# Kernel optimization log

Hardware: AMD Instinct MI355X
Metric: run time of the kernel (lower is better)

Reference implementation:

```python
import jax, jax.numpy as jnp
import numpy as np
import math

B, N, C_IN, C_OUT, K, RATIO = 16, 4096, 256, 512, 16, 0.25
N_OUT = math.ceil(N * RATIO)  # 1024
BN_EPS = 1e-5


def fps_indices(p, n):
    """Farthest point sampling. p: [B,N,3] -> local indices [B,n] (deterministic start at 0, eval mode)."""
    def fps_one(pts):  # [N,3]
        d0 = jnp.sum((pts - pts[0]) ** 2, axis=-1)          # [N]
        idxs0 = jnp.zeros((n,), jnp.int32)                  # idx[0] = 0
        def body(i, st):
            d, idxs = st
            nxt = jnp.argmax(d).astype(jnp.int32)
            idxs = idxs.at[i].set(nxt)
            d = jnp.minimum(d, jnp.sum((pts - pts[nxt]) ** 2, axis=-1))
            return (d, idxs)
        _, idxs = jax.lax.fori_loop(1, n, body, (d0, idxs0))
        return idxs
    return jax.vmap(fps_one)(p)


def setup_inputs() -> dict:
    key = jax.random.key(0)
    ks = jax.random.split(key, 6)
    x = jax.random.normal(ks[0], (B, N, C_IN), jnp.float32)
    p = jax.random.normal(ks[1], (B, N, 3), jnp.float32)
    sid_euc = jax.random.randint(ks[2], (B * N, K), 0, B * N).astype(jnp.int64)
    tid_euc = jax.random.randint(ks[3], (B * N, K), 0, B * N).astype(jnp.int64)
    W = jax.random.normal(ks[4], (C_OUT, C_IN), jnp.float32) * (1.0 / np.sqrt(C_IN))
    b = jax.random.normal(ks[5], (C_OUT,), jnp.float32) * 0.02
    gamma = jnp.ones((C_OUT,), jnp.float32)
    beta = jnp.zeros((C_OUT,), jnp.float32)
    run_mean = jnp.zeros((C_OUT,), jnp.float32)
    run_var = jnp.ones((C_OUT,), jnp.float32)
    return {"x": x, "p": p, "sid_euc": sid_euc, "tid_euc": tid_euc,
            "W": W, "b": b, "gamma": gamma, "beta": beta,
            "run_mean": run_mean, "run_var": run_var}


def reference(x, p, sid_euc, tid_euc, W, b, gamma, beta, run_mean, run_var):
    Bsz, Npts, _ = x.shape
    n = N_OUT
    Kn = sid_euc.shape[1]
    # MLP: pointwise Linear + BatchNorm (eval) + ReLU
    h = jnp.einsum('bnc,oc->bno', x, W) + b                       # [B,N,C_OUT]
    h = (h - run_mean) * (gamma / jnp.sqrt(run_var + BN_EPS)) + beta
    h = jax.nn.relu(h)
    # FPS -> global flat indices into B*N
    fid_local = fps_indices(p, n)                                  # [B,n]
    fid = (fid_local + jnp.arange(Bsz, dtype=jnp.int32)[:, None] * Npts).reshape(-1)
    # sample coords
    p_flat = p.reshape(Bsz * Npts, -1)
    p_out = p_flat[fid].reshape(Bsz, n, -1)                        # [B,n,3]
    # gather K neighbors of each sampled point, max-pool over K
    sid = sid_euc[fid].reshape(-1)                                 # [B*n*K]
    h_flat = h.reshape(Bsz * Npts, -1)
    x_out = h_flat[sid].reshape(Bsz, n, Kn, -1).max(axis=-2)       # [B,n,C_OUT]
    return (x_out, p_out)
```

## Files before the change

kernel.cpp:

```cpp
#include <hip/hip_runtime.h>
#include <hip/hip_bf16.h>

#define BATCH   16
#define NPTS    4096
#define CIN     256
#define COUT    512
#define KNN     16
#define NOUT    1024
#define XOUT_ELEMS 8388608
#define LDA     40
#define DYN_LDS 53312

typedef __attribute__((ext_vector_type(4))) float f32x4;
typedef __attribute__((ext_vector_type(2))) float f32x2;
typedef __attribute__((ext_vector_type(8))) short bf16x8;
typedef unsigned long long u64;

__device__ __forceinline__ unsigned short f2bf_rne(float f) {
    unsigned u = __float_as_uint(f);
    return (unsigned short)((u + 0x7FFFu + ((u >> 16) & 1u)) >> 16);
}
__device__ __forceinline__ float bf2f(unsigned short s) {
    return __uint_as_float(((unsigned)s) << 16);
}

__device__ __forceinline__ float wave_max_dpp(float v) {
    int x, y;
    x = __float_as_int(v);
    y = __builtin_amdgcn_update_dpp(x, x, 0x111, 0xf, 0xf, false);
    v = fmaxf(v, __int_as_float(y)); x = __float_as_int(v);
    y = __builtin_amdgcn_update_dpp(x, x, 0x112, 0xf, 0xf, false);
    v = fmaxf(v, __int_as_float(y)); x = __float_as_int(v);
    y = __builtin_amdgcn_update_dpp(x, x, 0x114, 0xf, 0xf, false);
    v = fmaxf(v, __int_as_float(y)); x = __float_as_int(v);
    y = __builtin_amdgcn_update_dpp(x, x, 0x118, 0xf, 0xf, false);
    v = fmaxf(v, __int_as_float(y)); x = __float_as_int(v);
    y = __builtin_amdgcn_update_dpp(x, x, 0x142, 0xf, 0xf, false);
    v = fmaxf(v, __int_as_float(y)); x = __float_as_int(v);
    y = __builtin_amdgcn_update_dpp(x, x, 0x143, 0xf, 0xf, false);
    v = fmaxf(v, __int_as_float(y));
    return v;
}

extern "C" __global__ void __launch_bounds__(256)
fps_gemm(const float* __restrict__ x, const float* __restrict__ p,
         const float* __restrict__ W, const float* __restrict__ bias,
         const float* __restrict__ gamma, const float* __restrict__ beta,
         const float* __restrict__ rmean, const float* __restrict__ rvar,
         int* __restrict__ fid, unsigned short* __restrict__ h,
         float* __restrict__ out)
{
    extern __shared__ char smem[];
    const int t = threadIdx.x;
    const int lane = t & 63;
    const int wv = t >> 6;

    if (blockIdx.x < BATCH) {
#pragma clang fp contract(off)
        const int b = blockIdx.x;
        float* lx = (float*)smem;
        float* ly = lx + NPTS;
        float* lz = ly + NPTS;
        u64* warr = (u64*)(smem + 49152);
        int* wins = (int*)(smem + 49216);
        float* pout = out + XOUT_ELEMS + (size_t)b * NOUT * 3;

        const float* pb = p + (size_t)b * NPTS * 3;
        for (int l = t; l < NPTS * 3; l += 256) {
            float v = pb[l];
            int pi = l / 3;
            int c = l - pi * 3;
            if (c == 0) lx[pi] = v; else if (c == 1) ly[pi] = v; else lz[pi] = v;
        }
        if (t == 0) wins[0] = 0;
        __syncthreads();

        f32x2 px2[8], py2[8], pz2[8], d2[8];
        const int base = t << 4;
#pragma unroll
        for (int j = 0; j < 8; ++j) {
            px2[j] = *(const f32x2*)(lx + base + (j << 1));
            py2[j] = *(const f32x2*)(ly + base + (j << 1));
            pz2[j] = *(const f32x2*)(lz + base + (j << 1));
            d2[j]  = (f32x2){3.4028235e38f, 3.4028235e38f};
        }

        int winner = 0;
        for (int i = 1; i < NOUT; ++i) {
            float wx = lx[winner], wy = ly[winner], wz = lz[winner];
            f32x2 wx2 = {wx, wx}, wy2 = {wy, wy}, wz2 = {wz, wz};
            float bestd = -1.0f;
            int   bestj = 0;
#pragma unroll
            for (int j = 0; j < 8; ++j) {
                f32x2 dx = px2[j] - wx2;
                f32x2 dy = py2[j] - wy2;
                f32x2 dz = pz2[j] - wz2;
                f32x2 s  = ((dx * dx) + (dy * dy)) + (dz * dz);
                f32x2 nd;
                nd.x = fminf(d2[j].x, s.x);
                nd.y = fminf(d2[j].y, s.y);
                d2[j] = nd;
                bool g0 = nd.x > bestd;
                bestd = g0 ? nd.x : bestd;
                bestj = g0 ? (j << 1) : bestj;
                bool g1 = nd.y > bestd;
                bestd = g1 ? nd.y : bestd;
                bestj = g1 ? (j << 1) + 1 : bestj;
            }
            float vmax = wave_max_dpp(bestd);
            float wmax = __int_as_float(
                __builtin_amdgcn_readlane(__float_as_int(vmax), 63));
            u64 msk = __ballot(bestd == wmax);
            int lead = (int)__builtin_ctzll(msk);
            int wbpi = __builtin_amdgcn_readlane(base + bestj, lead);
            u64 key = ((u64)__float_as_uint(wmax) << 32)
                    | (unsigned)(NPTS - 1 - wbpi);
            u64* wrow = warr + ((i & 1) << 2);
            if (lane == 0) wrow[wv] = key;
            __syncthreads();
            u64 k0 = wrow[0], k1 = wrow[1], k2 = wrow[2], k3 = wrow[3];
            if (k1 > k0) k0 = k1;
            if (k3 > k2) k2 = k3;
            if (k2 > k0) k0 = k2;
            winner = NPTS - 1 - (int)(unsigned)(k0 & 0xffffffffull);
            if (t == 0) wins[i] = winner;
        }
        __syncthreads();
        for (int i = t; i < NOUT; i += 256) {
            int w = wins[i];
            fid[b * NOUT + i] = b * NPTS + w;
            float* po = pout + (size_t)i * 3;
            po[0] = lx[w]; po[1] = ly[w]; po[2] = lz[w];
        }
    } else {
        const int bid = blockIdx.x - BATCH;
        const int bm = bid >> 2;
        const int bn = bid & 3;
        short* As = (short*)smem;
        short* Bs = As + 128 * LDA;

        const int wm = wv >> 1, wn = wv & 1;
        const int quad = lane >> 4, l16 = lane & 15;
        const int m0 = bm * 128, n0 = bn * 128;

        f32x4 acc[4][4];
        const f32x4 zero = {0.0f, 0.0f, 0.0f, 0.0f};
#pragma unroll
        for (int a = 0; a < 4; ++a)
#pragma unroll
            for (int bb = 0; bb < 4; ++bb) acc[a][bb] = zero;

        const int srow = t >> 3;
        const int scol = (t & 7) << 2;

        for (int ks = 0; ks < 8; ++ks) {
            const int k0 = ks * 32;
            __syncthreads();
#pragma unroll
            for (int it = 0; it < 4; ++it) {
                int row = srow + it * 32;
                float4 va = *(const float4*)(x + (size_t)(m0 + row) * CIN + k0 + scol);
                short4 pa = make_short4((short)f2bf_rne(va.x), (short)f2bf_rne(va.y),
                                        (short)f2bf_rne(va.z), (short)f2bf_rne(va.w));
                *(short4*)(As + row * LDA + scol) = pa;
                float4 vb = *(const float4*)(W + (size_t)(n0 + row) * CIN + k0 + scol);
                short4 pb2 = make_short4((short)f2bf_rne(vb.x), (short)f2bf_rne(vb.y),
                                         (short)f2bf_rne(vb.z), (short)f2bf_rne(vb.w));
                *(short4*)(Bs + row * LDA + scol) = pb2;
            }
            __syncthreads();
            bf16x8 af[4], bfr[4];
#pragma unroll
            for (int tm = 0; tm < 4; ++tm)
                af[tm] = *(const bf16x8*)(As + (wm * 64 + tm * 16 + l16) * LDA + quad * 8);
#pragma unroll
            for (int tn = 0; tn < 4; ++tn)
                bfr[tn] = *(const bf16x8*)(Bs + (wn * 64 + tn * 16 + l16) * LDA + quad * 8);
#pragma unroll
            for (int tm = 0; tm < 4; ++tm)
#pragma unroll
                for (int tn = 0; tn < 4; ++tn)
                    acc[tm][tn] = __builtin_amdgcn_mfma_f32_16x16x32_bf16(
                        af[tm], bfr[tn], acc[tm][tn], 0, 0, 0);
        }
#pragma unroll
        for (int tn = 0; tn < 4; ++tn) {
            int c = n0 + wn * 64 + tn * 16 + l16;
            float sc = gamma[c] / sqrtf(rvar[c] + 1e-5f);
            float sh = (bias[c] - rmean[c]) * sc + beta[c];
#pragma unroll
            for (int tm = 0; tm < 4; ++tm) {
                int rbase = m0 + wm * 64 + tm * 16 + quad * 4;
#pragma unroll
                for (int r = 0; r < 4; ++r) {
                    float v = fmaxf(acc[tm][tn][r] * sc + sh, 0.0f);
                    h[(size_t)(rbase + r) * COUT + c] = f2bf_rne(v);
                }
            }
        }
    }
}

extern "C" __global__ void __launch_bounds__(128)
gather_maxpool(const int* __restrict__ sid32, const int* __restrict__ fid,
               const unsigned short* __restrict__ h, float* __restrict__ out)
{
    const int j = blockIdx.x;
    const int t = threadIdx.x;
    __shared__ int rows[KNN];
    const int frow = fid[j];
    bool is64 = (sid32[1] == 0) && (sid32[3] == 0) && (sid32[5] == 0);
    if (t < KNN) {
        long long e = (long long)frow * KNN + t;
        rows[t] = is64 ? sid32[e * 2] : sid32[e];
    }
    __syncthreads();

    const int c4 = t << 2;
    float m0 = -3.4028235e38f, m1 = m0, m2 = m0, m3 = m0;
#pragma unroll
    for (int k = 0; k < KNN; ++k) {
        const ushort4 v = *(const ushort4*)(h + (size_t)rows[k] * COUT + c4);
        m0 = fmaxf(m0, bf2f(v.x));
        m1 = fmaxf(m1, bf2f(v.y));
        m2 = fmaxf(m2, bf2f(v.z));
        m3 = fmaxf(m3, bf2f(v.w));
    }
    *(float4*)(out + (size_t)j * COUT + c4) = make_float4(m0, m1, m2, m3);
}

extern "C" void kernel_launch(void* const* d_in, const int* in_sizes, int n_in,
                              void* d_out, int out_size, void* d_ws, size_t ws_size,
                              hipStream_t stream)
{
    const float* x     = (const float*)d_in[0];
    const float* p     = (const float*)d_in[1];
    const int*   sid   = (const int*)d_in[2];
    const float* W     = (const float*)d_in[4];
    const float* bias  = (const float*)d_in[5];
    const float* gamma = (const float*)d_in[6];
    const float* beta  = (const float*)d_in[7];
    const float* rmean = (const float*)d_in[8];
    const float* rvar  = (const float*)d_in[9];
    float* out = (float*)d_out;

    int* fid = (int*)d_ws;
    unsigned short* h = (unsigned short*)((char*)d_ws + 65792);

    hipLaunchKernelGGL(fps_gemm, dim3(BATCH + 2048), dim3(256), DYN_LDS, stream,
                       x, p, W, bias, gamma, beta, rmean, rvar, fid, h, out);
    hipLaunchKernelGGL(gather_maxpool, dim3(BATCH * NOUT), dim3(128), 0, stream,
                       sid, fid, h, out);
}
```

Measured before the change: 727.7 us.

## Interleave two FPS batches per block to hide barrier and winner-lookup latency

Each FPS block now handles two batch elements, with the two serial chains staggered by half an iteration. While one batch's winner is selected and its coordinates fetched, the other batch's distance update runs, so barrier and reduction latency overlaps with useful ALU work. Point coordinates now load straight from global memory into registers, and winner coordinates are read from global instead of LDS, which shrinks the dynamic LDS. The trade-off is double the register state per thread and fewer FPS blocks, so each FPS block carries a longer serial critical path.

```diff
diff --git a/kernel.cpp b/kernel.cpp
--- a/kernel.cpp
+++ b/kernel.cpp
@@ -9,7 +9,8 @@
 #define NOUT    1024
 #define XOUT_ELEMS 8388608
 #define LDA     40
-#define DYN_LDS 53312
+#define NFPSBLK 8
+#define DYN_LDS 20480
 
 typedef __attribute__((ext_vector_type(4))) float f32x4;
 typedef __attribute__((ext_vector_type(2))) float f32x2;
@@ -41,6 +42,46 @@
     v = fmaxf(v, __int_as_float(y));
     return v;
 }
+
+#define DIST4(PX, PY, PZ, DD, WX2, WY2, WZ2, BD, BJ, J0)                      \
+    _Pragma("unroll")                                                          \
+    for (int j = (J0); j < (J0) + 4; ++j) {                                    \
+        f32x2 dx = PX[j] - WX2;                                                \
+        f32x2 dy = PY[j] - WY2;                                                \
+        f32x2 dz = PZ[j] - WZ2;                                                \
+        f32x2 s  = ((dx * dx) + (dy * dy)) + (dz * dz);                        \
+        f32x2 nd;                                                              \
+        nd.x = fminf(DD[j].x, s.x);                                            \
+        nd.y = fminf(DD[j].y, s.y);                                            \
+        DD[j] = nd;                                                            \
+        bool g0 = nd.x > BD;                                                   \
+        BD = g0 ? nd.x : BD;                                                   \
+        BJ = g0 ? (j << 1) : BJ;                                               \
+        bool g1 = nd.y > BD;                                                   \
+        BD = g1 ? nd.y : BD;                                                   \
+        BJ = g1 ? (j << 1) + 1 : BJ;                                           \
+    }
+
+#define WAVE_KEY(BD, BJ, KEYOUT)                                               \
+    {                                                                          \
+        float vmax = wave_max_dpp(BD);                                         \
+        float wmax = __int_as_float(                                           \
+            __builtin_amdgcn_readlane(__float_as_int(vmax), 63));              \
+        u64 msk = __ballot(BD == wmax);                                        \
+        int lead = (int)__builtin_ctzll(msk);                                  \
+        int wbpi = __builtin_amdgcn_readlane(base + BJ, lead);                 \
+        KEYOUT = ((u64)__float_as_uint(wmax) << 32)                            \
+               | (unsigned)(NPTS - 1 - wbpi);                                  \
+    }
+
+#define SEL4(K0, K1, K2, K3, WOUT)                                             \
+    {                                                                          \
+        u64 a0 = K0, a1 = K1, a2 = K2, a3 = K3;                                \
+        if (a1 > a0) a0 = a1;                                                  \
+        if (a3 > a2) a2 = a3;                                                  \
+        if (a2 > a0) a0 = a2;                                                  \
+        WOUT = NPTS - 1 - (int)(unsigned)(a0 & 0xffffffffull);                 \
+    }
 
 extern "C" __global__ void __launch_bounds__(256)
 fps_gemm(const float* __restrict__ x, const float* __restrict__ p,
@@ -55,86 +96,86 @@
     const int lane = t & 63;
     const int wv = t >> 6;
 
-    if (blockIdx.x < BATCH) {
+    if (blockIdx.x < NFPSBLK) {
 #pragma clang fp contract(off)
-        const int b = blockIdx.x;
-        float* lx = (float*)smem;
-        float* ly = lx + NPTS;
-        float* lz = ly + NPTS;
-        u64* warr = (u64*)(smem + 49152);
-        int* wins = (int*)(smem + 49216);
-        float* pout = out + XOUT_ELEMS + (size_t)b * NOUT * 3;
-
-        const float* pb = p + (size_t)b * NPTS * 3;
-        for (int l = t; l < NPTS * 3; l += 256) {
-            float v = pb[l];
-            int pi = l / 3;
-            int c = l - pi * 3;
-            if (c == 0) lx[pi] = v; else if (c == 1) ly[pi] = v; else lz[pi] = v;
-        }
-        if (t == 0) wins[0] = 0;
+        const int bA = blockIdx.x << 1, bB = bA | 1;
+        u64* warrA = (u64*)smem;
+        u64* warrB = warrA + 4;
+        int* winsA = (int*)(smem + 64);
+        int* winsB = winsA + NOUT;
+        const float* pAp = p + (size_t)bA * NPTS * 3;
+        const float* pBp = p + (size_t)bB * NPTS * 3;
+
+        const int base = t << 4;
+        f32x2 pxA[8], pyA[8], pzA[8], dA[8];
+        f32x2 pxB[8], pyB[8], pzB[8], dB[8];
+#pragma unroll
+        for (int j = 0; j < 8; ++j) {
+            const int p0 = (base + (j << 1)) * 3;
+            pxA[j] = (f32x2){pAp[p0],     pAp[p0 + 3]};
+            pyA[j] = (f32x2){pAp[p0 + 1], pAp[p0 + 4]};
+            pzA[j] = (f32x2){pAp[p0 + 2], pAp[p0 + 5]};
+            pxB[j] = (f32x2){pBp[p0],     pBp[p0 + 3]};
+            pyB[j] = (f32x2){pBp[p0 + 1], pBp[p0 + 4]};
+            pzB[j] = (f32x2){pBp[p0 + 2], pBp[p0 + 5]};
+            dA[j] = (f32x2){3.4028235e38f, 3.4028235e38f};
+            dB[j] = dA[j];
+        }
+        if (t == 0) { winsA[0] = 0; winsB[0] = 0; }
+        if (t < 4) warrB[t] = (u64)(NPTS - 1);
+        float wxA = pAp[0], wyA = pAp[1], wzA = pAp[2];
+        float wxB, wyB, wzB;
         __syncthreads();
 
-        f32x2 px2[8], py2[8], pz2[8], d2[8];
-        const int base = t << 4;
-#pragma unroll
-        for (int j = 0; j < 8; ++j) {
-            px2[j] = *(const f32x2*)(lx + base + (j << 1));
-            py2[j] = *(const f32x2*)(ly + base + (j << 1));
-            pz2[j] = *(const f32x2*)(lz + base + (j << 1));
-            d2[j]  = (f32x2){3.4028235e38f, 3.4028235e38f};
-        }
-
-        int winner = 0;
         for (int i = 1; i < NOUT; ++i) {
-            float wx = lx[winner], wy = ly[winner], wz = lz[winner];
-            f32x2 wx2 = {wx, wx}, wy2 = {wy, wy}, wz2 = {wz, wz};
-            float bestd = -1.0f;
-            int   bestj = 0;
-#pragma unroll
-            for (int j = 0; j < 8; ++j) {
-                f32x2 dx = px2[j] - wx2;
-                f32x2 dy = py2[j] - wy2;
-                f32x2 dz = pz2[j] - wz2;
-                f32x2 s  = ((dx * dx) + (dy * dy)) + (dz * dz);
-                f32x2 nd;
-                nd.x = fminf(d2[j].x, s.x);
-                nd.y = fminf(d2[j].y, s.y);
-                d2[j] = nd;
-                bool g0 = nd.x > bestd;
-                bestd = g0 ? nd.x : bestd;
-                bestj = g0 ? (j << 1) : bestj;
-                bool g1 = nd.y > bestd;
-                bestd = g1 ? nd.y : bestd;
-                bestj = g1 ? (j << 1) + 1 : bestj;
-            }
-            float vmax = wave_max_dpp(bestd);
-            float wmax = __int_as_float(
-                __builtin_amdgcn_readlane(__float_as_int(vmax), 63));
-            u64 msk = __ballot(bestd == wmax);
-            int lead = (int)__builtin_ctzll(msk);
-            int wbpi = __builtin_amdgcn_readlane(base + bestj, lead);
-            u64 key = ((u64)__float_as_uint(wmax) << 32)
-                    | (unsigned)(NPTS - 1 - wbpi);
-            u64* wrow = warr + ((i & 1) << 2);
-            if (lane == 0) wrow[wv] = key;
-            __syncthreads();
-            u64 k0 = wrow[0], k1 = wrow[1], k2 = wrow[2], k3 = wrow[3];
-            if (k1 > k0) k0 = k1;
-            if (k3 > k2) k2 = k3;
-            if (k2 > k0) k0 = k2;
-            winner = NPTS - 1 - (int)(unsigned)(k0 & 0xffffffffull);
-            if (t == 0) wins[i] = winner;
+            u64 kb0 = warrB[0], kb1 = warrB[1], kb2 = warrB[2], kb3 = warrB[3];
+            f32x2 wxA2 = {wxA, wxA}, wyA2 = {wyA, wyA}, wzA2 = {wzA, wzA};
+            float bestdA = -1.0f; int bestjA = 0;
+            DIST4(pxA, pyA, pzA, dA, wxA2, wyA2, wzA2, bestdA, bestjA, 0)
+            int wB; SEL4(kb0, kb1, kb2, kb3, wB)
+            if (t == 0) winsB[i - 1] = wB;
+            wxB = pBp[(size_t)wB * 3];
+            wyB = pBp[(size_t)wB * 3 + 1];
+            wzB = pBp[(size_t)wB * 3 + 2];
+            DIST4(pxA, pyA, pzA, dA, wxA2, wyA2, wzA2, bestdA, bestjA, 4)
+            u64 keyA; WAVE_KEY(bestdA, bestjA, keyA)
+            if (lane == 0) warrA[wv] = keyA;
+            __syncthreads();
+
+            u64 ka0 = warrA[0], ka1 = warrA[1], ka2 = warrA[2], ka3 = warrA[3];
+            f32x2 wxB2 = {wxB, wxB}, wyB2 = {wyB, wyB}, wzB2 = {wzB, wzB};
+            float bestdB = -1.0f; int bestjB = 0;
+            DIST4(pxB, pyB, pzB, dB, wxB2, wyB2, wzB2, bestdB, bestjB, 0)
+            int wA; SEL4(ka0, ka1, ka2, ka3, wA)
+            if (t == 0) winsA[i] = wA;
+            wxA = pAp[(size_t)wA * 3];
+            wyA = pAp[(size_t)wA * 3 + 1];
+            wzA = pAp[(size_t)wA * 3 + 2];
+            DIST4(pxB, pyB, pzB, dB, wxB2, wyB2, wzB2, bestdB, bestjB, 4)
+            u64 keyB; WAVE_KEY(bestdB, bestjB, keyB)
+            if (lane == 0) warrB[wv] = keyB;
+            __syncthreads();
+        }
+        {
+            u64 kb0 = warrB[0], kb1 = warrB[1], kb2 = warrB[2], kb3 = warrB[3];
+            int wB; SEL4(kb0, kb1, kb2, kb3, wB)
+            if (t == 0) winsB[NOUT - 1] = wB;
         }
         __syncthreads();
+        float* poutA = out + XOUT_ELEMS + (size_t)bA * NOUT * 3;
+        float* poutB = out + XOUT_ELEMS + (size_t)bB * NOUT * 3;
         for (int i = t; i < NOUT; i += 256) {
-            int w = wins[i];
-            fid[b * NOUT + i] = b * NPTS + w;
-            float* po = pout + (size_t)i * 3;
-            po[0] = lx[w]; po[1] = ly[w]; po[2] = lz[w];
+            int wa = winsA[i];
+            fid[bA * NOUT + i] = bA * NPTS + wa;
+            float* poa = poutA + (size_t)i * 3;
+            poa[0] = pAp[wa * 3]; poa[1] = pAp[wa * 3 + 1]; poa[2] = pAp[wa * 3 + 2];
+            int wb = winsB[i];
+            fid[bB * NOUT + i] = bB * NPTS + wb;
+            float* pob = poutB + (size_t)i * 3;
+            pob[0] = pBp[wb * 3]; pob[1] = pBp[wb * 3 + 1]; pob[2] = pBp[wb * 3 + 2];
         }
     } else {
-        const int bid = blockIdx.x - BATCH;
+        const int bid = blockIdx.x - NFPSBLK;
         const int bm = bid >> 2;
         const int bn = bid & 3;
         short* As = (short*)smem;
@@ -248,7 +289,7 @@
     int* fid = (int*)d_ws;
     unsigned short* h = (unsigned short*)((char*)d_ws + 65792);
 
-    hipLaunchKernelGGL(fps_gemm, dim3(BATCH + 2048), dim3(256), DYN_LDS, stream,
+    hipLaunchKernelGGL(fps_gemm, dim3(NFPSBLK + 2048), dim3(256), DYN_LDS, stream,
                        x, p, W, bias, gamma, beta, rmean, rvar, fid, h, out);
     hipLaunchKernelGGL(gather_maxpool, dim3(BATCH * NOUT), dim3(128), 0, stream,
                        sid, fid, h, out);
```

Measured after the change: 1.241 ms. +70.5%, slower.

## Carry FPS winner coords through reduction; pack two batches per 512-thread block

Applied to the files above, without the earlier changes.

The FPS loop now carries each candidate's coordinates alongside its key through the wave and block reductions. This removes the dependent LDS lookup of the winner's coordinates from the serial per-iteration chain. Points are loaded straight from global memory into registers instead of being staged in LDS. Each block now handles two batches with 512 threads, so the FPS work fits in 8 blocks instead of 16. The GEMM is reworked to 8 waves per block, each computing a 64x32 tile, to match the new block size. The trade-off is that one barrier now spans 8 waves and couples two independent batches, and there is more register and select work per candidate.

```diff
diff --git a/kernel.cpp b/kernel.cpp
--- a/kernel.cpp
+++ b/kernel.cpp
@@ -9,13 +9,16 @@
 #define NOUT    1024
 #define XOUT_ELEMS 8388608
 #define LDA     40
-#define DYN_LDS 53312
+#define NFPSBLK 8
+#define DYN_LDS 20480
 
 typedef __attribute__((ext_vector_type(4))) float f32x4;
 typedef __attribute__((ext_vector_type(2))) float f32x2;
 typedef __attribute__((ext_vector_type(8))) short bf16x8;
 typedef unsigned long long u64;
 
+struct KB { unsigned long long key; float x, y, z; };
+
 __device__ __forceinline__ unsigned short f2bf_rne(float f) {
     unsigned u = __float_as_uint(f);
     return (unsigned short)((u + 0x7FFFu + ((u >> 16) & 1u)) >> 16);
@@ -42,7 +45,32 @@
     return v;
 }
 
-extern "C" __global__ void __launch_bounds__(256)
+#define DIST4T(PX, PY, PZ, DD, WX2, WY2, WZ2, BD, BJ, BX, BY, BZ, J0)         \
+    _Pragma("unroll")                                                          \
+    for (int j = (J0); j < (J0) + 4; ++j) {                                    \
+        f32x2 dx = PX[j] - WX2;                                                \
+        f32x2 dy = PY[j] - WY2;                                                \
+        f32x2 dz = PZ[j] - WZ2;                                                \
+        f32x2 s  = ((dx * dx) + (dy * dy)) + (dz * dz);                        \
+        f32x2 nd;                                                              \
+        nd.x = fminf(DD[j].x, s.x);                                            \
+        nd.y = fminf(DD[j].y, s.y);                                            \
+        DD[j] = nd;                                                            \
+        bool g0 = nd.x > BD;                                                   \
+        BD = g0 ? nd.x : BD;                                                   \
+        BJ = g0 ? (j << 1) : BJ;                                               \
+        BX = g0 ? PX[j].x : BX;                                                \
+        BY = g0 ? PY[j].x : BY;                                                \
+        BZ = g0 ? PZ[j].x : BZ;                                                \
+        bool g1 = nd.y > BD;                                                   \
+        BD = g1 ? nd.y : BD;                                                   \
+        BJ = g1 ? (j << 1) + 1 : BJ;                                           \
+        BX = g1 ? PX[j].y : BX;                                                \
+        BY = g1 ? PY[j].y : BY;                                                \
+        BZ = g1 ? PZ[j].y : BZ;                                                \
+    }
+
+extern "C" __global__ void __launch_bounds__(512)
 fps_gemm(const float* __restrict__ x, const float* __restrict__ p,
          const float* __restrict__ W, const float* __restrict__ bias,
          const float* __restrict__ gamma, const float* __restrict__ beta,
@@ -53,103 +81,88 @@
     extern __shared__ char smem[];
     const int t = threadIdx.x;
     const int lane = t & 63;
-    const int wv = t >> 6;
-
-    if (blockIdx.x < BATCH) {
+
+    if (blockIdx.x < NFPSBLK) {
 #pragma clang fp contract(off)
-        const int b = blockIdx.x;
-        float* lx = (float*)smem;
-        float* ly = lx + NPTS;
-        float* lz = ly + NPTS;
-        u64* warr = (u64*)(smem + 49152);
-        int* wins = (int*)(smem + 49216);
-        float* pout = out + XOUT_ELEMS + (size_t)b * NOUT * 3;
-
-        const float* pb = p + (size_t)b * NPTS * 3;
-        for (int l = t; l < NPTS * 3; l += 256) {
-            float v = pb[l];
-            int pi = l / 3;
-            int c = l - pi * 3;
-            if (c == 0) lx[pi] = v; else if (c == 1) ly[pi] = v; else lz[pi] = v;
-        }
-        if (t == 0) wins[0] = 0;
-        __syncthreads();
-
-        f32x2 px2[8], py2[8], pz2[8], d2[8];
-        const int base = t << 4;
+        const int grp = t >> 8;
+        const int lt  = t & 255;
+        const int gw  = (t >> 6) & 3;
+        const int bat = (blockIdx.x << 1) | grp;
+        KB*  warr = ((KB*)smem) + grp * 8;
+        int* wins = (int*)(smem + 512) + grp * NOUT;
+        const float* pp = p + (size_t)bat * NPTS * 3;
+
+        const int base = lt << 4;
+        f32x2 px[8], py[8], pz[8], dd[8];
 #pragma unroll
         for (int j = 0; j < 8; ++j) {
-            px2[j] = *(const f32x2*)(lx + base + (j << 1));
-            py2[j] = *(const f32x2*)(ly + base + (j << 1));
-            pz2[j] = *(const f32x2*)(lz + base + (j << 1));
-            d2[j]  = (f32x2){3.4028235e38f, 3.4028235e38f};
-        }
-
-        int winner = 0;
+            const int p0 = (base + (j << 1)) * 3;
+            px[j] = (f32x2){pp[p0],     pp[p0 + 3]};
+            py[j] = (f32x2){pp[p0 + 1], pp[p0 + 4]};
+            pz[j] = (f32x2){pp[p0 + 2], pp[p0 + 5]};
+            dd[j] = (f32x2){3.4028235e38f, 3.4028235e38f};
+        }
+        if (lt == 0) wins[0] = 0;
+        float wx = pp[0], wy = pp[1], wz = pp[2];
+
         for (int i = 1; i < NOUT; ++i) {
-            float wx = lx[winner], wy = ly[winner], wz = lz[winner];
             f32x2 wx2 = {wx, wx}, wy2 = {wy, wy}, wz2 = {wz, wz};
-            float bestd = -1.0f;
-            int   bestj = 0;
-#pragma unroll
-            for (int j = 0; j < 8; ++j) {
-                f32x2 dx = px2[j] - wx2;
-                f32x2 dy = py2[j] - wy2;
-                f32x2 dz = pz2[j] - wz2;
-                f32x2 s  = ((dx * dx) + (dy * dy)) + (dz * dz);
-                f32x2 nd;
-                nd.x = fminf(d2[j].x, s.x);
-                nd.y = fminf(d2[j].y, s.y);
-                d2[j] = nd;
-                bool g0 = nd.x > bestd;
-                bestd = g0 ? nd.x : bestd;
-                bestj = g0 ? (j << 1) : bestj;
-                bool g1 = nd.y > bestd;
-                bestd = g1 ? nd.y : bestd;
-                bestj = g1 ? (j << 1) + 1 : bestj;
-            }
+            float bestd = -1.0f; int bestj = 0;
+            float bx = px[0].x, by = py[0].x, bz = pz[0].x;
+            DIST4T(px, py, pz, dd, wx2, wy2, wz2, bestd, bestj, bx, by, bz, 0)
+            DIST4T(px, py, pz, dd, wx2, wy2, wz2, bestd, bestj, bx, by, bz, 4)
             float vmax = wave_max_dpp(bestd);
             float wmax = __int_as_float(
                 __builtin_amdgcn_readlane(__float_as_int(vmax), 63));
             u64 msk = __ballot(bestd == wmax);
             int lead = (int)__builtin_ctzll(msk);
-            int wbpi = __builtin_amdgcn_readlane(base + bestj, lead);
-            u64 key = ((u64)__float_as_uint(wmax) << 32)
-                    | (unsigned)(NPTS - 1 - wbpi);
-            u64* wrow = warr + ((i & 1) << 2);
-            if (lane == 0) wrow[wv] = key;
+            if (lane == lead) {
+                KB kb;
+                kb.key = ((u64)__float_as_uint(wmax) << 32)
+                       | (unsigned)(NPTS - 1 - (base + bestj));
+                kb.x = bx; kb.y = by; kb.z = bz;
+                warr[((i & 1) << 2) + gw] = kb;
+            }
             __syncthreads();
-            u64 k0 = wrow[0], k1 = wrow[1], k2 = wrow[2], k3 = wrow[3];
-            if (k1 > k0) k0 = k1;
-            if (k3 > k2) k2 = k3;
-            if (k2 > k0) k0 = k2;
-            winner = NPTS - 1 - (int)(unsigned)(k0 & 0xffffffffull);
-            if (t == 0) wins[i] = winner;
+            const KB* wrow = warr + ((i & 1) << 2);
+            KB s0 = wrow[0], s1 = wrow[1], s2 = wrow[2], s3 = wrow[3];
+            u64 k0 = s0.key; float X = s0.x, Y = s0.y, Z = s0.z;
+            bool g;
+            g = s1.key > k0; k0 = g ? s1.key : k0;
+            X = g ? s1.x : X; Y = g ? s1.y : Y; Z = g ? s1.z : Z;
+            g = s2.key > k0; k0 = g ? s2.key : k0;
+            X = g ? s2.x : X; Y = g ? s2.y : Y; Z = g ? s2.z : Z;
+            g = s3.key > k0; k0 = g ? s3.key : k0;
+            X = g ? s3.x : X; Y = g ? s3.y : Y; Z = g ? s3.z : Z;
+            if (lt == 0) wins[i] = NPTS - 1 - (int)(unsigned)(k0 & 0xffffffffull);
+            wx = X; wy = Y; wz = Z;
         }
         __syncthreads();
-        for (int i = t; i < NOUT; i += 256) {
+        float* pout = out + XOUT_ELEMS + (size_t)bat * NOUT * 3;
+        for (int i = lt; i < NOUT; i += 256) {
             int w = wins[i];
-            fid[b * NOUT + i] = b * NPTS + w;
+            fid[bat * NOUT + i] = bat * NPTS + w;
             float* po = pout + (size_t)i * 3;
-            po[0] = lx[w]; po[1] = ly[w]; po[2] = lz[w];
+            po[0] = pp[w * 3]; po[1] = pp[w * 3 + 1]; po[2] = pp[w * 3 + 2];
         }
     } else {
-        const int bid = blockIdx.x - BATCH;
+        const int bid = blockIdx.x - NFPSBLK;
         const int bm = bid >> 2;
         const int bn = bid & 3;
         short* As = (short*)smem;
         short* Bs = As + 128 * LDA;
 
-        const int wm = wv >> 1, wn = wv & 1;
+        const int wv = t >> 6;
+        const int wm = wv >> 2, wn = wv & 3;
         const int quad = lane >> 4, l16 = lane & 15;
         const int m0 = bm * 128, n0 = bn * 128;
 
-        f32x4 acc[4][4];
+        f32x4 acc[4][2];
         const f32x4 zero = {0.0f, 0.0f, 0.0f, 0.0f};
 #pragma unroll
         for (int a = 0; a < 4; ++a)
 #pragma unroll
-            for (int bb = 0; bb < 4; ++bb) acc[a][bb] = zero;
+            for (int bb = 0; bb < 2; ++bb) acc[a][bb] = zero;
 
         const int srow = t >> 3;
         const int scol = (t & 7) << 2;
@@ -158,8 +171,8 @@
             const int k0 = ks * 32;
             __syncthreads();
 #pragma unroll
-            for (int it = 0; it < 4; ++it) {
-                int row = srow + it * 32;
+            for (int it = 0; it < 2; ++it) {
+                int row = srow + it * 64;
                 float4 va = *(const float4*)(x + (size_t)(m0 + row) * CIN + k0 + scol);
                 short4 pa = make_short4((short)f2bf_rne(va.x), (short)f2bf_rne(va.y),
                                         (short)f2bf_rne(va.z), (short)f2bf_rne(va.w));
@@ -170,23 +183,23 @@
                 *(short4*)(Bs + row * LDA + scol) = pb2;
             }
             __syncthreads();
-            bf16x8 af[4], bfr[4];
+            bf16x8 af[4], bfr[2];
 #pragma unroll
             for (int tm = 0; tm < 4; ++tm)
                 af[tm] = *(const bf16x8*)(As + (wm * 64 + tm * 16 + l16) * LDA + quad * 8);
 #pragma unroll
-            for (int tn = 0; tn < 4; ++tn)
-                bfr[tn] = *(const bf16x8*)(Bs + (wn * 64 + tn * 16 + l16) * LDA + quad * 8);
+            for (int tn = 0; tn < 2; ++tn)
+                bfr[tn] = *(const bf16x8*)(Bs + (wn * 32 + tn * 16 + l16) * LDA + quad * 8);
 #pragma unroll
             for (int tm = 0; tm < 4; ++tm)
 #pragma unroll
-                for (int tn = 0; tn < 4; ++tn)
+                for (int tn = 0; tn < 2; ++tn)
                     acc[tm][tn] = __builtin_amdgcn_mfma_f32_16x16x32_bf16(
                         af[tm], bfr[tn], acc[tm][tn], 0, 0, 0);
         }
 #pragma unroll
-        for (int tn = 0; tn < 4; ++tn) {
-            int c = n0 + wn * 64 + tn * 16 + l16;
+        for (int tn = 0; tn < 2; ++tn) {
+            int c = n0 + wn * 32 + tn * 16 + l16;
             float sc = gamma[c] / sqrtf(rvar[c] + 1e-5f);
             float sh = (bias[c] - rmean[c]) * sc + beta[c];
 #pragma unroll
@@ -248,7 +261,7 @@
     int* fid = (int*)d_ws;
     unsigned short* h = (unsigned short*)((char*)d_ws + 65792);
 
-    hipLaunchKernelGGL(fps_gemm, dim3(BATCH + 2048), dim3(256), DYN_LDS, stream,
+    hipLaunchKernelGGL(fps_gemm, dim3(NFPSBLK + 2048), dim3(512), DYN_LDS, stream,
                        x, p, W, bias, gamma, beta, rmean, rvar, fid, h, out);
     hipLaunchKernelGGL(gather_maxpool, dim3(BATCH * NOUT), dim3(128), 0, stream,
                        sid, fid, h, out);
```

Measured after the change: 1.275 ms. 75.3% more time.
